# Optimization experiments

Measured on AMD Instinct MI355X. Metric: run time of the kernel, lower is better.

The kernel has to match this reference:

```python
import jax, jax.numpy as jnp
import numpy as np

EPS = 1e-12  # torch F.normalize eps

def _l2norm(v, axis):
    n = jnp.linalg.norm(v, axis=axis, keepdims=True)
    return v / jnp.maximum(n, EPS)

def setup_inputs() -> dict:
    key = jax.random.key(0)
    k1, k2, k3 = jax.random.split(key, 3)
    N, D, H, W, K = 32, 512, 40, 40, 64
    x = jax.random.normal(k1, (N, D, H, W), dtype=jnp.float32)
    conv_weight = jax.random.normal(k2, (K, D), dtype=jnp.float32) * 0.05
    centroids = jax.random.uniform(k3, (K, D), dtype=jnp.float32)
    return {"x": x, "conv_weight": conv_weight, "centroids": centroids}

def reference(x, conv_weight, centroids):
    N, D, H, W = x.shape
    K = centroids.shape[0]
    # descriptor-wise L2 normalization over channel dim
    x = _l2norm(x, axis=1)
    x_flat = x.reshape(N, D, H * W)                       # [N, D, S]
    # 1x1 conv == per-pixel linear: [K,D] @ [N,D,S] -> [N,K,S]
    logits = jnp.einsum('kd,nds->nks', conv_weight, x_flat)
    soft_assign = jax.nn.softmax(logits, axis=1)          # softmax over clusters
    # vlad[n,k,d] = sum_s a[n,k,s] * (x[n,d,s] - c[k,d])
    #            = (a @ x^T) - (sum_s a) * c   -- two GEMM-like ops, no K-loop
    agg = jnp.einsum('nks,nds->nkd', soft_assign, x_flat)  # [N, K, D]
    a_sum = soft_assign.sum(axis=2)                        # [N, K]
    vlad = agg - a_sum[:, :, None] * centroids[None, :, :]
    # intra-normalization over D, flatten, global L2 normalization
    vlad = _l2norm(vlad, axis=2)
    vlad = vlad.reshape(N, K * D)
    vlad = _l2norm(vlad, axis=1)
    return vlad
```

## Files before the change

kernel.cpp:

```cpp
#include <hip/hip_runtime.h>
#include <math.h>

#define N_ 32
#define D_ 512
#define S_ 1600
#define K_ 64

typedef __attribute__((ext_vector_type(8))) short short8;
typedef __attribute__((ext_vector_type(4))) float f32x4;

static __device__ __forceinline__ short f2bf(float f) {
    unsigned u = __float_as_uint(f);
    u += 0x7fffu + ((u >> 16) & 1u);
    return (short)(u >> 16);
}

__global__ __launch_bounds__(256) void kW(const float* __restrict__ w,
                                          short* __restrict__ w16)
{
    int i4 = (blockIdx.x * 256 + threadIdx.x) * 4;
    float4 v = *(const float4*)&w[i4];
    short4 h = {f2bf(v.x), f2bf(v.y), f2bf(v.z), f2bf(v.w)};
    *(short4*)&w16[i4] = h;
}

#define TP 72

__global__ __launch_bounds__(256) void kA(const float* __restrict__ x,
                                          const short* __restrict__ w16,
                                          short* __restrict__ aprime,
                                          float* __restrict__ asum)
{
    __shared__ short T[64 * TP];
    __shared__ float pssq[16 * 66];
    __shared__ float invL[64];
    __shared__ float wred[2][4][64];

    const int tid = threadIdx.x;
    const int n  = blockIdx.x / 25;
    const int s0 = (blockIdx.x % 25) * 64;
    const int wv = tid >> 6;
    const int l  = tid & 63;
    const int lk = l & 15;
    const int q  = l >> 4;

    const float* xb = x + (size_t)n * D_ * S_ + s0;
    const int sg = (tid & 15) * 4;
    const int dg = tid >> 4;

    f32x4 acc[4];
#pragma unroll
    for (int st = 0; st < 4; ++st) acc[st] = (f32x4){0.f, 0.f, 0.f, 0.f};
    float ssql[4] = {0.f, 0.f, 0.f, 0.f};

    for (int dc = 0; dc < D_; dc += 64) {
        __syncthreads();
#pragma unroll
        for (int j = 0; j < 4; ++j) {
            int dci = dg + 16 * j;
            float4 v = *(const float4*)&xb[(size_t)(dc + dci) * S_ + sg];
            ssql[0] += v.x * v.x;  ssql[1] += v.y * v.y;
            ssql[2] += v.z * v.z;  ssql[3] += v.w * v.w;
            T[(sg + 0) * TP + dci] = f2bf(v.x);
            T[(sg + 1) * TP + dci] = f2bf(v.y);
            T[(sg + 2) * TP + dci] = f2bf(v.z);
            T[(sg + 3) * TP + dci] = f2bf(v.w);
        }
        __syncthreads();

#pragma unroll
        for (int kst = 0; kst < 2; ++kst) {
            short8 af = *(const short8*)&w16[(16 * wv + lk) * D_ + dc + kst * 32 + q * 8];
#pragma unroll
            for (int st = 0; st < 4; ++st) {
                short8 bf = *(const short8*)&T[(st * 16 + lk) * TP + kst * 32 + q * 8];
                acc[st] = __builtin_amdgcn_mfma_f32_16x16x32_bf16(af, bf, acc[st], 0, 0, 0);
            }
        }
    }

    __syncthreads();
#pragma unroll
    for (int i = 0; i < 4; ++i) pssq[dg * 66 + sg + i] = ssql[i];
    __syncthreads();
    if (tid < 64) {
        float ss = 0.f;
#pragma unroll
        for (int g = 0; g < 16; ++g) ss += pssq[g * 66 + tid];
        invL[tid] = 1.0f / fmaxf(sqrtf(ss), 1e-12f);
    }
    __syncthreads();

    float lg[4][4], invv[4];
#pragma unroll
    for (int st = 0; st < 4; ++st) {
        invv[st] = invL[st * 16 + lk];
#pragma unroll
        for (int r = 0; r < 4; ++r) lg[st][r] = acc[st][r] * invv[st];
    }
    float mx[4];
#pragma unroll
    for (int st = 0; st < 4; ++st) {
        float m = fmaxf(fmaxf(lg[st][0], lg[st][1]), fmaxf(lg[st][2], lg[st][3]));
        m = fmaxf(m, __shfl_xor(m, 16));
        m = fmaxf(m, __shfl_xor(m, 32));
        mx[st] = m;
        if (q == 0) wred[0][wv][st * 16 + lk] = m;
    }
    __syncthreads();
    float gm[4];
#pragma unroll
    for (int st = 0; st < 4; ++st) {
        float m = wred[0][0][st * 16 + lk];
        m = fmaxf(m, wred[0][1][st * 16 + lk]);
        m = fmaxf(m, wred[0][2][st * 16 + lk]);
        m = fmaxf(m, wred[0][3][st * 16 + lk]);
        gm[st] = m;
    }
    float e[4][4];
#pragma unroll
    for (int st = 0; st < 4; ++st) {
        float s = 0.f;
#pragma unroll
        for (int r = 0; r < 4; ++r) {
            e[st][r] = __expf(lg[st][r] - gm[st]);
            s += e[st][r];
        }
        s += __shfl_xor(s, 16);
        s += __shfl_xor(s, 32);
        if (q == 0) wred[1][wv][st * 16 + lk] = s;
    }
    __syncthreads();
    float rs[4];
#pragma unroll
    for (int st = 0; st < 4; ++st) {
        float s = wred[1][0][st * 16 + lk] + wred[1][1][st * 16 + lk]
                + wred[1][2][st * 16 + lk] + wred[1][3][st * 16 + lk];
        rs[st] = 1.0f / s;
    }

    short* apb = aprime + (size_t)n * K_ * S_ + s0;
#pragma unroll
    for (int r = 0; r < 4; ++r) {
        const int k = 16 * wv + 4 * q + r;
        float accp = 0.f;
#pragma unroll
        for (int st = 0; st < 4; ++st) {
            float p = e[st][r] * rs[st];
            apb[(size_t)k * S_ + st * 16 + lk] = f2bf(p * invv[st]);
            accp += p;
        }
        accp += __shfl_xor(accp, 1);
        accp += __shfl_xor(accp, 2);
        accp += __shfl_xor(accp, 4);
        accp += __shfl_xor(accp, 8);
        if (lk == 0) atomicAdd(&asum[n * K_ + k], accp);
    }
}

__global__ __launch_bounds__(256) void kB(const float* __restrict__ x,
                                          const short* __restrict__ aprime,
                                          float* __restrict__ aggp)
{
    const int bid = blockIdx.x;
    const int n  = bid / 20;
    const int dt = (bid % 20) / 5;
    const int sp = bid % 5;
    const int wv = threadIdx.x >> 6;
    const int l  = threadIdx.x & 63;
    const int lk = l & 15;
    const int q  = l >> 4;
    const int dbase = dt * 128 + wv * 32;

    const short* ap = aprime + (size_t)n * K_ * S_;
    const float* xb = x + (size_t)n * D_ * S_;

    f32x4 acc[4][2];
#pragma unroll
    for (int kt = 0; kt < 4; ++kt)
#pragma unroll
        for (int ds = 0; ds < 2; ++ds) acc[kt][ds] = (f32x4){0.f, 0.f, 0.f, 0.f};

    for (int kst = 0; kst < 10; ++kst) {
        const int s = sp * 320 + kst * 32 + q * 8;
        short8 af[4];
#pragma unroll
        for (int kt = 0; kt < 4; ++kt)
            af[kt] = *(const short8*)&ap[(size_t)(kt * 16 + lk) * S_ + s];
        short8 bf[2];
#pragma unroll
        for (int ds = 0; ds < 2; ++ds) {
            const float* xp = &xb[(size_t)(dbase + ds * 16 + lk) * S_ + s];
            float4 v0 = *(const float4*)xp;
            float4 v1 = *(const float4*)(xp + 4);
            short8 b;
            b[0] = f2bf(v0.x); b[1] = f2bf(v0.y); b[2] = f2bf(v0.z); b[3] = f2bf(v0.w);
            b[4] = f2bf(v1.x); b[5] = f2bf(v1.y); b[6] = f2bf(v1.z); b[7] = f2bf(v1.w);
            bf[ds] = b;
        }
#pragma unroll
        for (int kt = 0; kt < 4; ++kt)
#pragma unroll
            for (int ds = 0; ds < 2; ++ds)
                acc[kt][ds] = __builtin_amdgcn_mfma_f32_16x16x32_bf16(af[kt], bf[ds], acc[kt][ds], 0, 0, 0);
    }

    float* ab = aggp + ((size_t)sp * N_ + n) * K_ * D_;
#pragma unroll
    for (int kt = 0; kt < 4; ++kt)
#pragma unroll
        for (int ds = 0; ds < 2; ++ds)
#pragma unroll
            for (int r = 0; r < 4; ++r)
                ab[(size_t)(kt * 16 + 4 * q + r) * D_ + dbase + ds * 16 + lk] = acc[kt][ds][r];
}

__global__ __launch_bounds__(256) void kC(const float* __restrict__ aggp,
                                          const float* __restrict__ asum,
                                          const float* __restrict__ cent,
                                          float* __restrict__ out)
{
    __shared__ float red[4];
    const int tid = threadIdx.x;
    const int nk = blockIdx.x;
    const int k = nk & 63;
    const float as = asum[nk];
    const float* cb = cent + (size_t)k * D_;

    float v0 = 0.f, v1 = 0.f;
#pragma unroll
    for (int p = 0; p < 5; ++p) {
        const float* ag = aggp + (size_t)p * N_ * K_ * D_ + (size_t)nk * D_;
        v0 += ag[tid];
        v1 += ag[tid + 256];
    }
    v0 -= as * cb[tid];
    v1 -= as * cb[tid + 256];
    float ssq = v0 * v0 + v1 * v1;

    ssq += __shfl_xor(ssq, 32);
    ssq += __shfl_xor(ssq, 16);
    ssq += __shfl_xor(ssq, 8);
    ssq += __shfl_xor(ssq, 4);
    ssq += __shfl_xor(ssq, 2);
    ssq += __shfl_xor(ssq, 1);
    if ((tid & 63) == 0) red[tid >> 6] = ssq;
    __syncthreads();
    const float total = red[0] + red[1] + red[2] + red[3];
    const float scale = 1.0f / (fmaxf(sqrtf(total), 1e-12f) * 8.0f);

    out[(size_t)nk * D_ + tid]       = v0 * scale;
    out[(size_t)nk * D_ + tid + 256] = v1 * scale;
}

extern "C" void kernel_launch(void* const* d_in, const int* in_sizes, int n_in,
                              void* d_out, int out_size, void* d_ws, size_t ws_size,
                              hipStream_t stream)
{
    const float* x    = (const float*)d_in[0];
    const float* w    = (const float*)d_in[1];
    const float* cent = (const float*)d_in[2];
    float* out = (float*)d_out;

    float* aggp   = (float*)d_ws;
    float* asum   = aggp + (size_t)5 * N_ * K_ * D_;
    short* aprime = (short*)(asum + N_ * K_);
    short* w16    = aprime + (size_t)N_ * K_ * S_;

    hipMemsetAsync(asum, 0, (size_t)N_ * K_ * sizeof(float), stream);

    kW<<<32, 256, 0, stream>>>(w, w16);
    kA<<<N_ * (S_ / 64), 256, 0, stream>>>(x, w16, aprime, asum);
    kB<<<N_ * 4 * 5, 256, 0, stream>>>(x, aprime, aggp);
    kC<<<N_ * K_, 256, 0, stream>>>(aggp, asum, cent, out);
}
```

Before: 203.5 us.

## Precompute bf16 and transposed bf16 copies of x in a separate pass

Adds a kernel that converts x to bf16 in both its native and a transposed [S,D] layout and writes per-tile partial sums of squares. The logits kernel then reads the transposed bf16 rows directly with no LDS staging or block syncs, computing softmax per wave. The aggregation kernel reads bf16 x instead of converting fp32 on the fly. In exchange this adds an extra launch and writes two bf16 copies of x to workspace, which raises total memory traffic.

```diff
diff --git a/kernel.cpp b/kernel.cpp
--- a/kernel.cpp
+++ b/kernel.cpp
@@ -24,141 +24,144 @@
     *(short4*)&w16[i4] = h;
 }
 
-#define TP 72
-
-__global__ __launch_bounds__(256) void kA(const float* __restrict__ x,
-                                          const short* __restrict__ w16,
+__global__ __launch_bounds__(256) void kX(const float* __restrict__ x,
+                                          short* __restrict__ x16,
+                                          short* __restrict__ xT16,
+                                          float* __restrict__ ssqp)
+{
+    __shared__ float tile[64 * 65];
+    const int bid = blockIdx.x;
+    const int n  = bid / 200;
+    const int dt = (bid % 200) / 25;
+    const int st = bid % 25;
+    const int d0 = dt * 64, s0 = st * 64;
+
+    const int lk = threadIdx.x & 15;
+    const int dg = threadIdx.x >> 4;
+    const int sg = lk * 4;
+
+    const float* xb = x + ((size_t)n * D_ + d0) * S_ + s0;
+    short* x16b = x16 + ((size_t)n * D_ + d0) * S_ + s0;
+
+#pragma unroll
+    for (int j = 0; j < 4; ++j) {
+        int row = dg + 16 * j;
+        float4 v = *(const float4*)&xb[(size_t)row * S_ + sg];
+        short4 h = {f2bf(v.x), f2bf(v.y), f2bf(v.z), f2bf(v.w)};
+        *(short4*)&x16b[(size_t)row * S_ + sg] = h;
+        tile[row * 65 + sg + 0] = v.x;
+        tile[row * 65 + sg + 1] = v.y;
+        tile[row * 65 + sg + 2] = v.z;
+        tile[row * 65 + sg + 3] = v.w;
+    }
+    __syncthreads();
+
+    const int srow = threadIdx.x >> 2;
+    const int dseg = (threadIdx.x & 3) * 16;
+    float ss = 0.f;
+    short8 o0, o1;
+#pragma unroll
+    for (int u = 0; u < 8; ++u) {
+        float v = tile[(dseg + u) * 65 + srow];
+        ss += v * v;
+        o0[u] = f2bf(v);
+    }
+#pragma unroll
+    for (int u = 0; u < 8; ++u) {
+        float v = tile[(dseg + 8 + u) * 65 + srow];
+        ss += v * v;
+        o1[u] = f2bf(v);
+    }
+    short* op = xT16 + ((size_t)n * S_ + s0 + srow) * D_ + d0 + dseg;
+    *(short8*)op = o0;
+    *(short8*)(op + 8) = o1;
+
+    ss += __shfl_xor(ss, 1);
+    ss += __shfl_xor(ss, 2);
+    if ((threadIdx.x & 3) == 0)
+        ssqp[((size_t)n * 8 + dt) * S_ + s0 + srow] = ss;
+}
+
+__global__ __launch_bounds__(256) void kA(const short* __restrict__ w16,
+                                          const short* __restrict__ xT16,
+                                          const float* __restrict__ ssqp,
                                           short* __restrict__ aprime,
                                           float* __restrict__ asum)
 {
-    __shared__ short T[64 * TP];
-    __shared__ float pssq[16 * 66];
-    __shared__ float invL[64];
-    __shared__ float wred[2][4][64];
-
-    const int tid = threadIdx.x;
     const int n  = blockIdx.x / 25;
     const int s0 = (blockIdx.x % 25) * 64;
-    const int wv = tid >> 6;
-    const int l  = tid & 63;
+    const int wv = threadIdx.x >> 6;
+    const int l  = threadIdx.x & 63;
     const int lk = l & 15;
     const int q  = l >> 4;
-
-    const float* xb = x + (size_t)n * D_ * S_ + s0;
-    const int sg = (tid & 15) * 4;
-    const int dg = tid >> 4;
+    const int s  = s0 + wv * 16 + lk;
+
+    const short* xr = xT16 + ((size_t)n * S_ + s) * D_;
 
     f32x4 acc[4];
 #pragma unroll
-    for (int st = 0; st < 4; ++st) acc[st] = (f32x4){0.f, 0.f, 0.f, 0.f};
-    float ssql[4] = {0.f, 0.f, 0.f, 0.f};
-
-    for (int dc = 0; dc < D_; dc += 64) {
-        __syncthreads();
-#pragma unroll
-        for (int j = 0; j < 4; ++j) {
-            int dci = dg + 16 * j;
-            float4 v = *(const float4*)&xb[(size_t)(dc + dci) * S_ + sg];
-            ssql[0] += v.x * v.x;  ssql[1] += v.y * v.y;
-            ssql[2] += v.z * v.z;  ssql[3] += v.w * v.w;
-            T[(sg + 0) * TP + dci] = f2bf(v.x);
-            T[(sg + 1) * TP + dci] = f2bf(v.y);
-            T[(sg + 2) * TP + dci] = f2bf(v.z);
-            T[(sg + 3) * TP + dci] = f2bf(v.w);
+    for (int kt = 0; kt < 4; ++kt) acc[kt] = (f32x4){0.f, 0.f, 0.f, 0.f};
+
+#pragma unroll
+    for (int dc = 0; dc < D_; dc += 32) {
+        short8 bf = *(const short8*)&xr[dc + q * 8];
+#pragma unroll
+        for (int kt = 0; kt < 4; ++kt) {
+            short8 af = *(const short8*)&w16[(kt * 16 + lk) * D_ + dc + q * 8];
+            acc[kt] = __builtin_amdgcn_mfma_f32_16x16x32_bf16(af, bf, acc[kt], 0, 0, 0);
         }
-        __syncthreads();
-
-#pragma unroll
-        for (int kst = 0; kst < 2; ++kst) {
-            short8 af = *(const short8*)&w16[(16 * wv + lk) * D_ + dc + kst * 32 + q * 8];
-#pragma unroll
-            for (int st = 0; st < 4; ++st) {
-                short8 bf = *(const short8*)&T[(st * 16 + lk) * TP + kst * 32 + q * 8];
-                acc[st] = __builtin_amdgcn_mfma_f32_16x16x32_bf16(af, bf, acc[st], 0, 0, 0);
-            }
+    }
+
+    float ssv = 0.f;
+#pragma unroll
+    for (int dt = 0; dt < 8; ++dt) ssv += ssqp[((size_t)n * 8 + dt) * S_ + s];
+    const float inv = 1.0f / fmaxf(sqrtf(ssv), 1e-12f);
+
+    float lg[4][4];
+#pragma unroll
+    for (int kt = 0; kt < 4; ++kt)
+#pragma unroll
+        for (int r = 0; r < 4; ++r) lg[kt][r] = acc[kt][r] * inv;
+
+    float m = -1e30f;
+#pragma unroll
+    for (int kt = 0; kt < 4; ++kt)
+#pragma unroll
+        for (int r = 0; r < 4; ++r) m = fmaxf(m, lg[kt][r]);
+    m = fmaxf(m, __shfl_xor(m, 16));
+    m = fmaxf(m, __shfl_xor(m, 32));
+
+    float e[4][4];
+    float sum = 0.f;
+#pragma unroll
+    for (int kt = 0; kt < 4; ++kt)
+#pragma unroll
+        for (int r = 0; r < 4; ++r) {
+            e[kt][r] = __expf(lg[kt][r] - m);
+            sum += e[kt][r];
         }
-    }
-
-    __syncthreads();
-#pragma unroll
-    for (int i = 0; i < 4; ++i) pssq[dg * 66 + sg + i] = ssql[i];
-    __syncthreads();
-    if (tid < 64) {
-        float ss = 0.f;
-#pragma unroll
-        for (int g = 0; g < 16; ++g) ss += pssq[g * 66 + tid];
-        invL[tid] = 1.0f / fmaxf(sqrtf(ss), 1e-12f);
-    }
-    __syncthreads();
-
-    float lg[4][4], invv[4];
-#pragma unroll
-    for (int st = 0; st < 4; ++st) {
-        invv[st] = invL[st * 16 + lk];
-#pragma unroll
-        for (int r = 0; r < 4; ++r) lg[st][r] = acc[st][r] * invv[st];
-    }
-    float mx[4];
-#pragma unroll
-    for (int st = 0; st < 4; ++st) {
-        float m = fmaxf(fmaxf(lg[st][0], lg[st][1]), fmaxf(lg[st][2], lg[st][3]));
-        m = fmaxf(m, __shfl_xor(m, 16));
-        m = fmaxf(m, __shfl_xor(m, 32));
-        mx[st] = m;
-        if (q == 0) wred[0][wv][st * 16 + lk] = m;
-    }
-    __syncthreads();
-    float gm[4];
-#pragma unroll
-    for (int st = 0; st < 4; ++st) {
-        float m = wred[0][0][st * 16 + lk];
-        m = fmaxf(m, wred[0][1][st * 16 + lk]);
-        m = fmaxf(m, wred[0][2][st * 16 + lk]);
-        m = fmaxf(m, wred[0][3][st * 16 + lk]);
-        gm[st] = m;
-    }
-    float e[4][4];
-#pragma unroll
-    for (int st = 0; st < 4; ++st) {
-        float s = 0.f;
+    sum += __shfl_xor(sum, 16);
+    sum += __shfl_xor(sum, 32);
+    const float rs = 1.0f / sum;
+
+    short* apb = aprime + (size_t)n * K_ * S_;
+#pragma unroll
+    for (int kt = 0; kt < 4; ++kt)
 #pragma unroll
         for (int r = 0; r < 4; ++r) {
-            e[st][r] = __expf(lg[st][r] - gm[st]);
-            s += e[st][r];
+            const int k = kt * 16 + 4 * q + r;
+            float p = e[kt][r] * rs;
+            apb[(size_t)k * S_ + s] = f2bf(p * inv);
+            float t = p;
+            t += __shfl_xor(t, 1);
+            t += __shfl_xor(t, 2);
+            t += __shfl_xor(t, 4);
+            t += __shfl_xor(t, 8);
+            if (lk == 0) atomicAdd(&asum[n * K_ + k], t);
         }
-        s += __shfl_xor(s, 16);
-        s += __shfl_xor(s, 32);
-        if (q == 0) wred[1][wv][st * 16 + lk] = s;
-    }
-    __syncthreads();
-    float rs[4];
-#pragma unroll
-    for (int st = 0; st < 4; ++st) {
-        float s = wred[1][0][st * 16 + lk] + wred[1][1][st * 16 + lk]
-                + wred[1][2][st * 16 + lk] + wred[1][3][st * 16 + lk];
-        rs[st] = 1.0f / s;
-    }
-
-    short* apb = aprime + (size_t)n * K_ * S_ + s0;
-#pragma unroll
-    for (int r = 0; r < 4; ++r) {
-        const int k = 16 * wv + 4 * q + r;
-        float accp = 0.f;
-#pragma unroll
-        for (int st = 0; st < 4; ++st) {
-            float p = e[st][r] * rs[st];
-            apb[(size_t)k * S_ + st * 16 + lk] = f2bf(p * invv[st]);
-            accp += p;
-        }
-        accp += __shfl_xor(accp, 1);
-        accp += __shfl_xor(accp, 2);
-        accp += __shfl_xor(accp, 4);
-        accp += __shfl_xor(accp, 8);
-        if (lk == 0) atomicAdd(&asum[n * K_ + k], accp);
-    }
-}
-
-__global__ __launch_bounds__(256) void kB(const float* __restrict__ x,
+}
+
+__global__ __launch_bounds__(256) void kB(const short* __restrict__ x16,
                                           const short* __restrict__ aprime,
                                           float* __restrict__ aggp)
 {
@@ -173,7 +176,7 @@
     const int dbase = dt * 128 + wv * 32;
 
     const short* ap = aprime + (size_t)n * K_ * S_;
-    const float* xb = x + (size_t)n * D_ * S_;
+    const short* xb = x16 + (size_t)n * D_ * S_;
 
     f32x4 acc[4][2];
 #pragma unroll
@@ -189,15 +192,8 @@
             af[kt] = *(const short8*)&ap[(size_t)(kt * 16 + lk) * S_ + s];
         short8 bf[2];
 #pragma unroll
-        for (int ds = 0; ds < 2; ++ds) {
-            const float* xp = &xb[(size_t)(dbase + ds * 16 + lk) * S_ + s];
-            float4 v0 = *(const float4*)xp;
-            float4 v1 = *(const float4*)(xp + 4);
-            short8 b;
-            b[0] = f2bf(v0.x); b[1] = f2bf(v0.y); b[2] = f2bf(v0.z); b[3] = f2bf(v0.w);
-            b[4] = f2bf(v1.x); b[5] = f2bf(v1.y); b[6] = f2bf(v1.z); b[7] = f2bf(v1.w);
-            bf[ds] = b;
-        }
+        for (int ds = 0; ds < 2; ++ds)
+            bf[ds] = *(const short8*)&xb[(size_t)(dbase + ds * 16 + lk) * S_ + s];
 #pragma unroll
         for (int kt = 0; kt < 4; ++kt)
 #pragma unroll
@@ -264,13 +260,17 @@
 
     float* aggp   = (float*)d_ws;
     float* asum   = aggp + (size_t)5 * N_ * K_ * D_;
-    short* aprime = (short*)(asum + N_ * K_);
+    float* ssqp   = asum + (size_t)N_ * K_;
+    short* aprime = (short*)(ssqp + (size_t)N_ * 8 * S_);
     short* w16    = aprime + (size_t)N_ * K_ * S_;
+    short* x16    = w16 + (size_t)K_ * D_;
+    short* xT16   = x16 + (size_t)N_ * D_ * S_;
 
     hipMemsetAsync(asum, 0, (size_t)N_ * K_ * sizeof(float), stream);
 
     kW<<<32, 256, 0, stream>>>(w, w16);
-    kA<<<N_ * (S_ / 64), 256, 0, stream>>>(x, w16, aprime, asum);
-    kB<<<N_ * 4 * 5, 256, 0, stream>>>(x, aprime, aggp);
+    kX<<<N_ * 8 * 25, 256, 0, stream>>>(x, x16, xT16, ssqp);
+    kA<<<N_ * (S_ / 64), 256, 0, stream>>>(w16, xT16, ssqp, aprime, asum);
+    kB<<<N_ * 4 * 5, 256, 0, stream>>>(x16, aprime, aggp);
     kC<<<N_ * K_, 256, 0, stream>>>(aggp, asum, cent, out);
 }
```

Result: slower. 250.2 us (+23.0%).

## Cache bf16 copy of x in kA and split kB over more S chunks

Applied to the files above, without the earlier changes.

kA now writes a bf16 copy of x to workspace while it loads x, and kB reads that half-size copy instead of re-reading and converting the fp32 x. The kA load pattern changes to per-lane scalar loads with pairs packed into LDS (new padding), and kB's S-split goes from 5 to 10 partitions, doubling the grid and the partial-sum buffer that kC reduces. The aim is to cut kB's global traffic and conversion work and raise its parallelism. The cost is an extra 52MB write in kA, scalar rather than vector loads there, and more partial sums for kC to read.

```diff
diff --git a/kernel.cpp b/kernel.cpp
--- a/kernel.cpp
+++ b/kernel.cpp
@@ -24,15 +24,14 @@
     *(short4*)&w16[i4] = h;
 }
 
-#define TP 72
-
 __global__ __launch_bounds__(256) void kA(const float* __restrict__ x,
                                           const short* __restrict__ w16,
+                                          short* __restrict__ x16,
                                           short* __restrict__ aprime,
                                           float* __restrict__ asum)
 {
-    __shared__ short T[64 * TP];
-    __shared__ float pssq[16 * 66];
+    __shared__ short T[64 * 68];
+    __shared__ float pssq[4][64];
     __shared__ float invL[64];
     __shared__ float wred[2][4][64];
 
@@ -44,27 +43,28 @@
     const int lk = l & 15;
     const int q  = l >> 4;
 
-    const float* xb = x + (size_t)n * D_ * S_ + s0;
-    const int sg = (tid & 15) * 4;
-    const int dg = tid >> 4;
+    const float* xb = x + (size_t)n * D_ * S_ + s0 + l;
+    short* x16b = x16 + (size_t)n * D_ * S_ + s0 + l;
 
     f32x4 acc[4];
 #pragma unroll
     for (int st = 0; st < 4; ++st) acc[st] = (f32x4){0.f, 0.f, 0.f, 0.f};
-    float ssql[4] = {0.f, 0.f, 0.f, 0.f};
+    float ssl = 0.f;
 
     for (int dc = 0; dc < D_; dc += 64) {
         __syncthreads();
 #pragma unroll
-        for (int j = 0; j < 4; ++j) {
-            int dci = dg + 16 * j;
-            float4 v = *(const float4*)&xb[(size_t)(dc + dci) * S_ + sg];
-            ssql[0] += v.x * v.x;  ssql[1] += v.y * v.y;
-            ssql[2] += v.z * v.z;  ssql[3] += v.w * v.w;
-            T[(sg + 0) * TP + dci] = f2bf(v.x);
-            T[(sg + 1) * TP + dci] = f2bf(v.y);
-            T[(sg + 2) * TP + dci] = f2bf(v.z);
-            T[(sg + 3) * TP + dci] = f2bf(v.w);
+        for (int t = 0; t < 8; ++t) {
+            const int r = wv + 4 * t;
+            float v0 = xb[(size_t)(dc + 2 * r) * S_];
+            float v1 = xb[(size_t)(dc + 2 * r + 1) * S_];
+            ssl += v0 * v0 + v1 * v1;
+            unsigned lo = (unsigned short)f2bf(v0);
+            unsigned hi = (unsigned short)f2bf(v1);
+            unsigned p = lo | (hi << 16);
+            ((unsigned*)T)[l * 34 + r] = p;
+            x16b[(size_t)(dc + 2 * r) * S_]     = (short)lo;
+            x16b[(size_t)(dc + 2 * r + 1) * S_] = (short)hi;
         }
         __syncthreads();
 
@@ -73,20 +73,20 @@
             short8 af = *(const short8*)&w16[(16 * wv + lk) * D_ + dc + kst * 32 + q * 8];
 #pragma unroll
             for (int st = 0; st < 4; ++st) {
-                short8 bf = *(const short8*)&T[(st * 16 + lk) * TP + kst * 32 + q * 8];
+                const short* bp = &T[(st * 16 + lk) * 68 + kst * 32 + q * 8];
+                short4 b0 = *(const short4*)bp;
+                short4 b1 = *(const short4*)(bp + 4);
+                short8 bf = {b0.x, b0.y, b0.z, b0.w, b1.x, b1.y, b1.z, b1.w};
                 acc[st] = __builtin_amdgcn_mfma_f32_16x16x32_bf16(af, bf, acc[st], 0, 0, 0);
             }
         }
     }
 
     __syncthreads();
-#pragma unroll
-    for (int i = 0; i < 4; ++i) pssq[dg * 66 + sg + i] = ssql[i];
+    pssq[wv][l] = ssl;
     __syncthreads();
     if (tid < 64) {
-        float ss = 0.f;
-#pragma unroll
-        for (int g = 0; g < 16; ++g) ss += pssq[g * 66 + tid];
+        float ss = pssq[0][tid] + pssq[1][tid] + pssq[2][tid] + pssq[3][tid];
         invL[tid] = 1.0f / fmaxf(sqrtf(ss), 1e-12f);
     }
     __syncthreads();
@@ -158,14 +158,14 @@
     }
 }
 
-__global__ __launch_bounds__(256) void kB(const float* __restrict__ x,
+__global__ __launch_bounds__(256) void kB(const short* __restrict__ x16,
                                           const short* __restrict__ aprime,
                                           float* __restrict__ aggp)
 {
     const int bid = blockIdx.x;
-    const int n  = bid / 20;
-    const int dt = (bid % 20) / 5;
-    const int sp = bid % 5;
+    const int n  = bid / 40;
+    const int dt = (bid % 40) / 10;
+    const int sp = bid % 10;
     const int wv = threadIdx.x >> 6;
     const int l  = threadIdx.x & 63;
     const int lk = l & 15;
@@ -173,7 +173,7 @@
     const int dbase = dt * 128 + wv * 32;
 
     const short* ap = aprime + (size_t)n * K_ * S_;
-    const float* xb = x + (size_t)n * D_ * S_;
+    const short* xb = x16 + (size_t)n * D_ * S_;
 
     f32x4 acc[4][2];
 #pragma unroll
@@ -181,23 +181,17 @@
 #pragma unroll
         for (int ds = 0; ds < 2; ++ds) acc[kt][ds] = (f32x4){0.f, 0.f, 0.f, 0.f};
 
-    for (int kst = 0; kst < 10; ++kst) {
-        const int s = sp * 320 + kst * 32 + q * 8;
+#pragma unroll
+    for (int kst = 0; kst < 5; ++kst) {
+        const int s = sp * 160 + kst * 32 + q * 8;
         short8 af[4];
 #pragma unroll
         for (int kt = 0; kt < 4; ++kt)
             af[kt] = *(const short8*)&ap[(size_t)(kt * 16 + lk) * S_ + s];
         short8 bf[2];
 #pragma unroll
-        for (int ds = 0; ds < 2; ++ds) {
-            const float* xp = &xb[(size_t)(dbase + ds * 16 + lk) * S_ + s];
-            float4 v0 = *(const float4*)xp;
-            float4 v1 = *(const float4*)(xp + 4);
-            short8 b;
-            b[0] = f2bf(v0.x); b[1] = f2bf(v0.y); b[2] = f2bf(v0.z); b[3] = f2bf(v0.w);
-            b[4] = f2bf(v1.x); b[5] = f2bf(v1.y); b[6] = f2bf(v1.z); b[7] = f2bf(v1.w);
-            bf[ds] = b;
-        }
+        for (int ds = 0; ds < 2; ++ds)
+            bf[ds] = *(const short8*)&xb[(size_t)(dbase + ds * 16 + lk) * S_ + s];
 #pragma unroll
         for (int kt = 0; kt < 4; ++kt)
 #pragma unroll
@@ -229,7 +223,7 @@
 
     float v0 = 0.f, v1 = 0.f;
 #pragma unroll
-    for (int p = 0; p < 5; ++p) {
+    for (int p = 0; p < 10; ++p) {
         const float* ag = aggp + (size_t)p * N_ * K_ * D_ + (size_t)nk * D_;
         v0 += ag[tid];
         v1 += ag[tid + 256];
@@ -263,14 +257,15 @@
     float* out = (float*)d_out;
 
     float* aggp   = (float*)d_ws;
-    float* asum   = aggp + (size_t)5 * N_ * K_ * D_;
+    float* asum   = aggp + (size_t)10 * N_ * K_ * D_;
     short* aprime = (short*)(asum + N_ * K_);
     short* w16    = aprime + (size_t)N_ * K_ * S_;
+    short* x16    = w16 + (size_t)K_ * D_;
 
     hipMemsetAsync(asum, 0, (size_t)N_ * K_ * sizeof(float), stream);
 
     kW<<<32, 256, 0, stream>>>(w, w16);
-    kA<<<N_ * (S_ / 64), 256, 0, stream>>>(x, w16, aprime, asum);
-    kB<<<N_ * 4 * 5, 256, 0, stream>>>(x, aprime, aggp);
+    kA<<<N_ * (S_ / 64), 256, 0, stream>>>(x, w16, x16, aprime, asum);
+    kB<<<N_ * 4 * 10, 256, 0, stream>>>(x16, aprime, aggp);
     kC<<<N_ * K_, 256, 0, stream>>>(aggp, asum, cent, out);
 }
```

New measurement: 207.8 us. 2.1% more time.
